# Performance work log

Measured on AMD Instinct MI355X. Metric: run time of the kernel, lower is better.

## Reference

```python
import jax, jax.numpy as jnp
import numpy as np

SEGMENT_LENGTHS = (768, 1536, 3072, 6144, 12288)
DILATED_RATIOS = (1, 2, 4, 8, 16)
NUM_HEADS = 12
NEG_INF = -1e9


def _layer_norm(x, g, b, eps=1e-5):
    mu = jnp.mean(x, axis=-1, keepdims=True)
    var = jnp.mean((x - mu) ** 2, axis=-1, keepdims=True)
    return (x - mu) * jax.lax.rsqrt(var + eps) * g + b


def _dilated_branch(q, k, v, w, r):
    # q,k,v: (B, L, H, Dh); segment length w, dilation ratio r (w % r == 0)
    B, L, H, Dh = q.shape
    Lp = -(-L // w) * w
    n, m = Lp // w, w // r
    gsz = -(-H // r)  # head-group size (heads padded up to a multiple of r in LongNet)
    offs = jnp.arange(H) // gsz  # per-head token offset within each r-block
    oh = jax.nn.one_hot(offs, r, dtype=q.dtype)  # (H, r)

    def gather(t):
        t = jnp.pad(t, ((0, 0), (0, Lp - L), (0, 0), (0, 0)))
        t = t.reshape(B, n, m, r, H, Dh)  # segments of w = m blocks of r
        return jnp.einsum('bnmrhd,hr->bnmhd', t, oh)  # each head picks its offset

    qi, ki, vi = gather(q), gather(k), gather(v)
    s = jnp.einsum('bnihd,bnjhd->bnhij', qi * (Dh ** -0.5), ki)  # (B,n,H,m,m)
    lse = jax.scipy.special.logsumexp(s, axis=-1)  # (B,n,H,m)
    o = jnp.einsum('bnhij,bnjhd->bnihd', jax.nn.softmax(s, axis=-1), vi)
    # scatter back to dense token positions; uncovered slots get 0 / -inf lse
    o_full = jnp.einsum('bnmhd,hr->bnmrhd', o, oh).reshape(B, Lp, H, Dh)
    lse = jnp.transpose(lse, (0, 1, 3, 2))  # (B,n,m,H)
    lse_full = jnp.where(oh.T[None, None, None] > 0, lse[:, :, :, None, :], NEG_INF)
    lse_full = lse_full.reshape(B, Lp, H)
    return o_full[:, :L], lse_full[:, :L]


def _dilated_attention(q, k, v):
    outs, lses = [], []
    for w, r in zip(SEGMENT_LENGTHS, DILATED_RATIOS):
        o, l = _dilated_branch(q, k, v, w, r)
        outs.append(o)
        lses.append(l)
    lse = jnp.stack(lses)  # (n_branch, B, L, H)
    wts = jnp.exp(lse - lse.max(0))
    wts = wts / wts.sum(0)  # softmax-combine branches by their lse (LongNet recombination)
    return (jnp.stack(outs) * wts[..., None]).sum(0)  # (B, L, H, Dh)


def _forward(x, patch_w, patch_b, cls_token, pos_embed,
             ln1_g, ln1_b, wq, bq, wk, bk, wv, bv, wo, bo,
             ln2_g, ln2_b, w1, b1, w2, b2, normf_g, normf_b, head_w, head_b):
    B, Cin, D, Hs, Ws = x.shape
    E = patch_w.shape[0]
    pd, ph, pw = patch_w.shape[2], patch_w.shape[3], patch_w.shape[4]
    # non-overlapping 3D patch embed (Conv3d with stride == kernel)
    xp = x.reshape(B, Cin, D // pd, pd, Hs // ph, ph, Ws // pw, pw)
    tok = jnp.einsum('bcxpyqzr,ecpqr->bxyze', xp, patch_w).reshape(B, -1, E) + patch_b
    tok = tok + pos_embed[:, 1:]
    cls = cls_token + pos_embed[:, :1]
    h = jnp.concatenate([jnp.broadcast_to(cls, (B, 1, E)), tok], axis=1)
    L = h.shape[1]
    Dh = E // NUM_HEADS
    depth = wq.shape[0]
    for i in range(depth):  # pre-LN transformer layers with LongNet dilated attention
        hn = _layer_norm(h, ln1_g[i], ln1_b[i])
        q = (hn @ wq[i] + bq[i]).reshape(B, L, NUM_HEADS, Dh)
        k = (hn @ wk[i] + bk[i]).reshape(B, L, NUM_HEADS, Dh)
        v = (hn @ wv[i] + bv[i]).reshape(B, L, NUM_HEADS, Dh)
        a = _dilated_attention(q, k, v).reshape(B, L, E)
        h = h + a @ wo[i] + bo[i]
        hn = _layer_norm(h, ln2_g[i], ln2_b[i])
        h = h + jax.nn.gelu(hn @ w1[i] + b1[i], approximate=False) @ w2[i] + b2[i]
    h = _layer_norm(h, normf_g, normf_b)
    return h[:, 0] @ head_w + head_b  # (B, num_classes)


def setup_inputs() -> dict:
    key = jax.random.key(0)
    ks = jax.random.split(key, 12)
    B, E, depth, ncls = 2, 768, 2, 1000
    D, Hs, Ws = 48, 256, 256
    N = (D // 4) * (Hs // 16) * (Ws // 16)  # 3072 patches
    f32 = jnp.float32
    s = 0.02
    return {
        'x': jax.random.normal(ks[0], (B, 1, D, Hs, Ws), f32),
        'patch_w': jax.random.normal(ks[1], (E, 1, 4, 16, 16), f32) * s,
        'patch_b': jnp.zeros((E,), f32),
        'cls_token': jax.random.normal(ks[2], (1, 1, E), f32) * s,
        'pos_embed': jax.random.normal(ks[3], (1, N + 1, E), f32) * s,
        'ln1_g': jnp.ones((depth, E), f32),
        'ln1_b': jnp.zeros((depth, E), f32),
        'wq': jax.random.normal(ks[4], (depth, E, E), f32) * s,
        'bq': jnp.zeros((depth, E), f32),
        'wk': jax.random.normal(ks[5], (depth, E, E), f32) * s,
        'bk': jnp.zeros((depth, E), f32),
        'wv': jax.random.normal(ks[6], (depth, E, E), f32) * s,
        'bv': jnp.zeros((depth, E), f32),
        'wo': jax.random.normal(ks[7], (depth, E, E), f32) * s,
        'bo': jnp.zeros((depth, E), f32),
        'ln2_g': jnp.ones((depth, E), f32),
        'ln2_b': jnp.zeros((depth, E), f32),
        'w1': jax.random.normal(ks[8], (depth, E, 4 * E), f32) * s,
        'b1': jnp.zeros((depth, 4 * E), f32),
        'w2': jax.random.normal(ks[9], (depth, 4 * E, E), f32) * s,
        'b2': jnp.zeros((depth, E), f32),
        'normf_g': jnp.ones((E,), f32),
        'normf_b': jnp.zeros((E,), f32),
        'head_w': jax.random.normal(ks[10], (E, ncls), f32) * s,
        'head_b': jnp.zeros((ncls,), f32),
    }


def reference(x, patch_w, patch_b, cls_token, pos_embed,
              ln1_g, ln1_b, wq, bq, wk, bk, wv, bv, wo, bo,
              ln2_g, ln2_b, w1, b1, w2, b2, normf_g, normf_b, head_w, head_b):
    return _forward(x, patch_w, patch_b, cls_token, pos_embed,
                    ln1_g, ln1_b, wq, bq, wk, bk, wv, bv, wo, bo,
                    ln2_g, ln2_b, w1, b1, w2, b2, normf_g, normf_b, head_w, head_b)
```

## Files before the change

kernel.cpp:

```cpp
#include <hip/hip_runtime.h>
#include <math.h>

#define TOK_L 3073
#define EMB 768
#define NH 12
#define DH 64
#define BATCH 2
#define QKVS 2304
#define HSZ ((size_t)BATCH * TOK_L * EMB)
#define MHC ((size_t)BATCH * TOK_L * NH)

typedef __bf16 bf16;
typedef __bf16 v8bf __attribute__((ext_vector_type(8)));
typedef __bf16 v4bf __attribute__((ext_vector_type(4)));
typedef float  v4f  __attribute__((ext_vector_type(4)));

__device__ __forceinline__ v8bf zero8() {
    v8bf v;
    #pragma unroll
    for (int i = 0; i < 8; i++) v[i] = (bf16)0.f;
    return v;
}
__device__ __forceinline__ v4f zero4() {
    v4f v; v[0] = 0.f; v[1] = 0.f; v[2] = 0.f; v[3] = 0.f; return v;
}
__device__ __forceinline__ float gelu_f(float x) {
    return 0.5f * x * (1.0f + erff(x * 0.70710678118654752f));
}
__device__ __forceinline__ void gload16(const bf16* g, bf16* l) {
    __builtin_amdgcn_global_load_lds(
        (const __attribute__((address_space(1))) void*)g,
        (__attribute__((address_space(3))) void*)l, 16, 0, 0);
}

__device__ __forceinline__ void convT_tile(const float* __restrict__ src,
                                           bf16* __restrict__ dst,
                                           int K, int N, int tx, int ty)
{
    __shared__ float t[32][33];
    int n0 = tx * 32, k0 = ty * 32;
    int r = threadIdx.x >> 3, c4 = (threadIdx.x & 7) * 4;
    float4 v = *(const float4*)(src + (size_t)(k0 + r) * N + n0 + c4);
    t[r][c4 + 0] = v.x; t[r][c4 + 1] = v.y; t[r][c4 + 2] = v.z; t[r][c4 + 3] = v.w;
    __syncthreads();
    v4bf o;
    o[0] = (bf16)t[c4 + 0][r]; o[1] = (bf16)t[c4 + 1][r];
    o[2] = (bf16)t[c4 + 2][r]; o[3] = (bf16)t[c4 + 3][r];
    *(v4bf*)(dst + (size_t)(n0 + r) * K + k0 + c4) = o;
}

__global__ __launch_bounds__(256) void prep_weights(
    const float* __restrict__ wq, const float* __restrict__ wk,
    const float* __restrict__ wv, const float* __restrict__ wo,
    const float* __restrict__ w1, const float* __restrict__ w2,
    const float* __restrict__ patch_w,
    bf16* __restrict__ qkv_t0, bf16* __restrict__ wo_t0,
    bf16* __restrict__ w1_t, bf16* __restrict__ w2_t, bf16* __restrict__ pw_b)
{
    int bid = blockIdx.x;
    if (bid >= 13824) {
        int i = ((bid - 13824) * 256 + threadIdx.x) * 4;
        float4 v = *(const float4*)(patch_w + i);
        v4bf o; o[0] = (bf16)v.x; o[1] = (bf16)v.y; o[2] = (bf16)v.z; o[3] = (bf16)v.w;
        *(v4bf*)(pw_b + i) = o;
        return;
    }
    int layer = bid / 6912, t = bid % 6912;
    if (t < 1728) {
        int m = t / 576, tt = t % 576;
        const float* src = (m == 0 ? wq : m == 1 ? wk : wv) + (size_t)layer * 589824;
        bf16* dst = qkv_t0 + (size_t)layer * QKVS * 768 + (size_t)m * 589824;
        convT_tile(src, dst, 768, 768, tt % 24, tt / 24);
    } else if (t < 2304) {
        int tt = t - 1728;
        convT_tile(wo + (size_t)layer * 589824, wo_t0 + (size_t)layer * 589824,
                   768, 768, tt % 24, tt / 24);
    } else if (t < 4608) {
        int tt = t - 2304;
        convT_tile(w1 + (size_t)layer * 2359296, w1_t + (size_t)layer * 2359296,
                   768, 3072, tt % 96, tt / 96);
    } else {
        int tt = t - 4608;
        convT_tile(w2 + (size_t)layer * 2359296, w2_t + (size_t)layer * 2359296,
                   3072, 768, tt % 24, tt / 24);
    }
}

__global__ __launch_bounds__(256) void prep_small(const float* __restrict__ bq,
    const float* __restrict__ bk, const float* __restrict__ bv, float* __restrict__ d,
    const float* __restrict__ cls, const float* __restrict__ pos, float* __restrict__ h)
{
    int i = blockIdx.x * 256 + threadIdx.x;
    if (i < 2 * QKVS) {
        int layer = i / QKVS, j = i % QKVS;
        const float* s = (j < 768) ? bq : (j < 1536) ? bk : bv;
        d[i] = s[(size_t)layer * 768 + (j & 767)];
    }
    if (i < 2 * 768) {
        int b = i / 768, e = i % 768;
        h[(size_t)b * TOK_L * EMB + e] = cls[e] + pos[e];
    }
}

__global__ __launch_bounds__(256) void gather_patches(const float* __restrict__ x,
                                                      bf16* __restrict__ Xp) {
    int p = blockIdx.x;
    int b = p / 3072, pp = p % 3072;
    int px = pp >> 8, py = (pp >> 4) & 15, pz = pp & 15;
    for (int k = threadIdx.x; k < 1024; k += 256) {
        int pd = k >> 8, ph = (k >> 4) & 15, pw = k & 15;
        size_t src = ((size_t)(b * 48 + px * 4 + pd)) * 65536
                   + (size_t)(py * 16 + ph) * 256 + (size_t)(pz * 16 + pw);
        Xp[(size_t)p * 1024 + k] = (bf16)x[src];
    }
}

template<int BN>
__global__ __launch_bounds__(256) void gemm_bf16(
    const bf16* __restrict__ A, const bf16* __restrict__ Bt,
    const float* __restrict__ bias, float* __restrict__ Cf,
    bf16* __restrict__ Cb, int M, int N, int K, int flags,
    const float* __restrict__ pos)
{
    __shared__ bf16 As[128 * 32];
    __shared__ bf16 Bs[BN * 32];
    const int tid = threadIdx.x;
    const int lane = tid & 63, wid = tid >> 6;
    const int ln15 = lane & 15, q4 = lane >> 4;
    const int m0 = blockIdx.y * 128, n0 = blockIdx.x * BN;
    const int wm = (wid & 1) * 64, wn = (wid >> 1) * (BN / 2);
    const int srow = lane >> 2;
    const int schunk = (lane & 3) * 8;
    const int NF = BN / 32;

    v4f acc[4][NF];
    #pragma unroll
    for (int i = 0; i < 4; i++)
        #pragma unroll
        for (int j = 0; j < NF; j++) acc[i][j] = zero4();

    for (int k0 = 0; k0 < K; k0 += 32) {
        #pragma unroll
        for (int i = 0; i < 2; i++) {
            int rg = wid * 32 + i * 16;
            int gm = m0 + rg + srow; if (gm >= M) gm = M - 1;
            gload16(A + (size_t)gm * K + k0 + schunk, As + rg * 32);
        }
        if (BN == 128) {
            #pragma unroll
            for (int i = 0; i < 2; i++) {
                int rg = wid * 32 + i * 16;
                gload16(Bt + (size_t)(n0 + rg + srow) * K + k0 + schunk, Bs + rg * 32);
            }
        } else {
            int rg = wid * 16;
            gload16(Bt + (size_t)(n0 + rg + srow) * K + k0 + schunk, Bs + rg * 32);
        }
        __syncthreads();
        v8bf af[4], bfr[NF];
        #pragma unroll
        for (int mt = 0; mt < 4; mt++)
            af[mt] = *(const v8bf*)(As + (wm + mt * 16 + ln15) * 32 + q4 * 8);
        #pragma unroll
        for (int nt = 0; nt < NF; nt++)
            bfr[nt] = *(const v8bf*)(Bs + (wn + nt * 16 + ln15) * 32 + q4 * 8);
        #pragma unroll
        for (int mt = 0; mt < 4; mt++)
            #pragma unroll
            for (int nt = 0; nt < NF; nt++)
                acc[mt][nt] = __builtin_amdgcn_mfma_f32_16x16x32_bf16(af[mt], bfr[nt], acc[mt][nt], 0, 0, 0);
        __syncthreads();
    }
    #pragma unroll
    for (int mt = 0; mt < 4; mt++) {
        #pragma unroll
        for (int nt = 0; nt < NF; nt++) {
            #pragma unroll
            for (int g = 0; g < 4; g++) {
                int row = m0 + wm + mt * 16 + q4 * 4 + g;
                if (row >= M) continue;
                int col = n0 + wn + nt * 16 + ln15;
                float v = acc[mt][nt][g] + bias[col];
                if (flags & 2) v = gelu_f(v);
                size_t crow;
                if (flags & 4) {
                    int rowp = row % 3072;
                    crow = (size_t)(row + row / 3072 + 1);
                    v += pos[(size_t)(rowp + 1) * EMB + col];
                } else crow = (size_t)row;
                size_t ci = crow * (size_t)N + col;
                if (flags & 8) Cb[ci] = (bf16)v;
                else { if (flags & 1) v += Cf[ci]; Cf[ci] = v; }
            }
        }
    }
}

__global__ __launch_bounds__(256) void layernorm_kernel(
    const float* __restrict__ x, const float* __restrict__ g,
    const float* __restrict__ bb, bf16* __restrict__ y, int nrows)
{
    int row = blockIdx.x;
    if (row >= nrows) return;
    int tid = threadIdx.x;
    const float* xr = x + (size_t)row * EMB;
    float v0 = xr[tid], v1 = xr[tid + 256], v2 = xr[tid + 512];
    __shared__ float red[256];
    red[tid] = v0 + v1 + v2;
    __syncthreads();
    for (int o = 128; o > 0; o >>= 1) { if (tid < o) red[tid] += red[tid + o]; __syncthreads(); }
    float mu = red[0] * (1.f / 768.f);
    __syncthreads();
    float d0 = v0 - mu, d1 = v1 - mu, d2 = v2 - mu;
    red[tid] = d0 * d0 + d1 * d1 + d2 * d2;
    __syncthreads();
    for (int o = 128; o > 0; o >>= 1) { if (tid < o) red[tid] += red[tid + o]; __syncthreads(); }
    float rs = rsqrtf(red[0] * (1.f / 768.f) + 1e-5f);
    bf16* yr = y + (size_t)row * EMB;
    yr[tid]       = (bf16)(d0 * rs * g[tid]       + bb[tid]);
    yr[tid + 256] = (bf16)(d1 * rs * g[tid + 256] + bb[tid + 256]);
    yr[tid + 512] = (bf16)(d2 * rs * g[tid + 512] + bb[tid + 512]);
}

__global__ __launch_bounds__(256) void pack_vt(const bf16* __restrict__ qkv,
                                               bf16* __restrict__ Vt)
{
    __shared__ bf16 t[64 * 65];
    int yy = blockIdx.y;
    int br, seg;
    if (yy < 5)       { br = 0; seg = yy; }
    else if (yy < 8)  { br = 1; seg = yy - 5; }
    else if (yy < 10) { br = 2; seg = yy - 8; }
    else if (yy == 10){ br = 3; seg = 0; }
    else              { br = 4; seg = 0; }
    const int r = 1 << br, w = 768 << br;
    const int gsz = (NH + r - 1) / r;
    const int bh = blockIdx.z;
    const int b = bh / NH, hd = bh % NH;
    const int off = hd / gsz;
    const int kbase = seg * w + off;
    const int kt = blockIdx.x;
    const int tid = threadIdx.x;
    const int dq = (tid & 7) * 8;
    #pragma unroll
    for (int p = 0; p < 2; p++) {
        int jl = (tid >> 3) + p * 32;
        int pk = kbase + (kt * 64 + jl) * r;
        v8bf val = (pk < TOK_L)
            ? *(const v8bf*)(qkv + (size_t)(b * TOK_L + pk) * QKVS + 1536 + hd * DH + dq)
            : zero8();
        #pragma unroll
        for (int i = 0; i < 8; i++) t[jl * 65 + dq + i] = val[i];
    }
    __syncthreads();
    #pragma unroll
    for (int p = 0; p < 2; p++) {
        int d = (tid >> 3) + p * 32;
        int kk = (tid & 7) * 8;
        v8bf o;
        #pragma unroll
        for (int i = 0; i < 8; i++) o[i] = t[(kk + i) * 65 + d];
        *(v8bf*)(Vt + ((size_t)(yy * 24 + bh) * 64 + d) * 768 + kt * 64 + kk) = o;
    }
}

__global__ __launch_bounds__(256) void attn_mfma(
    const bf16* __restrict__ qkv, const bf16* __restrict__ Vt,
    bf16* __restrict__ oac, bf16* __restrict__ obr, float* __restrict__ lse5)
{
    __shared__ bf16 kl[2 * 4096];
    __shared__ bf16 pl[4][32 * 72];
    const int tid = threadIdx.x;
    const int lane = tid & 63, wid = tid >> 6;
    const int ln15 = lane & 15, q4 = lane >> 4;
    const int bid = blockIdx.x;
    const int xcd = bid & 7, rest = bid >> 3;
    const int slot = rest / 6, t = rest - slot * 6;
    const int g = (slot << 3) | xcd;
    const int yy = g / 24, bh = g - yy * 24;
    int br, seg;
    if (yy < 5)       { br = 0; seg = yy; }
    else if (yy < 8)  { br = 1; seg = yy - 5; }
    else if (yy < 10) { br = 2; seg = yy - 8; }
    else if (yy == 10){ br = 3; seg = 0; }
    else              { br = 4; seg = 0; }
    const int r = 1 << br, w = 768 << br;
    const int gsz = (NH + r - 1) / r;
    const int b = bh / NH, hd = bh % NH;
    const int off = hd / gsz;
    const int sbase = seg * w + off;
    if (sbase + (t * 128) * r >= TOK_L) return;

    int n_valid = (TOK_L - sbase + r - 1) / r;
    if (n_valid > 768) n_valid = 768;
    const int kt_lim = (n_valid + 63) >> 6;
    const float pad_add = (float)(768 - n_valid);
    const int qoff = t * 128 + wid * 32;
    const bool wactive = (sbase + qoff * r) < TOK_L;

    const bf16* qb_ = qkv + hd * DH;
    const bf16* kb_ = qkv + 768 + hd * DH;

    auto stageK = [&](int ktv, int bufi) {
        #pragma unroll
        for (int p = 0; p < 2; p++) {
            int row = (tid >> 3) + p * 32;
            int pk = sbase + (ktv * 64 + row) * r;
            if (pk >= TOK_L) pk = 0;
            gload16(kb_ + (size_t)(b * TOK_L + pk) * QKVS + (tid & 7) * 8,
                    kl + bufi * 4096 + wid * 512 + p * 2048);
        }
    };

    v8bf qf[2][2];
    #pragma unroll
    for (int mt = 0; mt < 2; mt++) {
        int pq = sbase + (qoff + mt * 16 + ln15) * r;
        #pragma unroll
        for (int ks = 0; ks < 2; ks++) {
            v8bf qv = (pq < TOK_L)
                ? *(const v8bf*)(qb_ + (size_t)(b * TOK_L + pq) * QKVS + ks * 32 + q4 * 8)
                : zero8();
            #pragma unroll
            for (int i = 0; i < 8; i++) qv[i] = (bf16)((float)qv[i] * 0.125f);
            qf[mt][ks] = qv;
        }
    }
    v4f o[2][4];
    float lsum[2][4];
    #pragma unroll
    for (int mt = 0; mt < 2; mt++)
        #pragma unroll
        for (int g2 = 0; g2 < 4; g2++) { lsum[mt][g2] = 0.f; o[mt][g2] = zero4(); }
    #pragma unroll
    for (int mt = 0; mt < 2; mt++)
        #pragma unroll
        for (int dt = 0; dt < 4; dt++) o[mt][dt] = zero4();

    const bf16* vtb = Vt + (size_t)(yy * 24 + bh) * 64 * 768;
    bf16* plw = &pl[wid][0];

    stageK(0, 0);
    __syncthreads();

    for (int kt = 0; kt < kt_lim; kt++) {
        const int cur = kt & 1;
        if (kt + 1 < kt_lim) stageK(kt + 1, cur ^ 1);
        if (wactive) {
            const bf16* klc = kl + cur * 4096;
            v8bf kf[4][2];
            #pragma unroll
            for (int nt = 0; nt < 4; nt++)
                #pragma unroll
                for (int ks = 0; ks < 2; ks++)
                    kf[nt][ks] = *(const v8bf*)(klc + (nt * 16 + ln15) * 64 + ks * 32 + q4 * 8);
            v4f s[2][4];
            #pragma unroll
            for (int mt = 0; mt < 2; mt++)
                #pragma unroll
                for (int nt = 0; nt < 4; nt++) {
                    s[mt][nt] = __builtin_amdgcn_mfma_f32_16x16x32_bf16(qf[mt][0], kf[nt][0], zero4(), 0, 0, 0);
                    s[mt][nt] = __builtin_amdgcn_mfma_f32_16x16x32_bf16(qf[mt][1], kf[nt][1], s[mt][nt], 0, 0, 0);
                }
            bool vm[4];
            #pragma unroll
            for (int nt = 0; nt < 4; nt++)
                vm[nt] = (kt * 64 + nt * 16 + ln15) < n_valid;
            #pragma unroll
            for (int mt = 0; mt < 2; mt++) {
                #pragma unroll
                for (int g2 = 0; g2 < 4; g2++) {
                    int rowq = mt * 16 + q4 * 4 + g2;
                    #pragma unroll
                    for (int nt = 0; nt < 4; nt++) {
                        float p = vm[nt] ? __expf(s[mt][nt][g2]) : 0.f;
                        lsum[mt][g2] += p;
                        plw[rowq * 72 + nt * 16 + ln15] = (bf16)p;
                    }
                }
            }
            #pragma unroll
            for (int ks = 0; ks < 2; ks++) {
                v8bf pa[2], vf[4];
                #pragma unroll
                for (int mt = 0; mt < 2; mt++)
                    pa[mt] = *(const v8bf*)(plw + (mt * 16 + ln15) * 72 + ks * 32 + q4 * 8);
                #pragma unroll
                for (int dt = 0; dt < 4; dt++)
                    vf[dt] = *(const v8bf*)(vtb + (size_t)(dt * 16 + ln15) * 768 + kt * 64 + ks * 32 + q4 * 8);
                #pragma unroll
                for (int mt = 0; mt < 2; mt++)
                    #pragma unroll
                    for (int dt = 0; dt < 4; dt++)
                        o[mt][dt] = __builtin_amdgcn_mfma_f32_16x16x32_bf16(pa[mt], vf[dt], o[mt][dt], 0, 0, 0);
            }
        }
        __syncthreads();
    }
    if (!wactive) return;

    bf16* od = (br == 0) ? oac : obr + (size_t)(br - 1) * HSZ;
    #pragma unroll
    for (int mt = 0; mt < 2; mt++) {
        #pragma unroll
        for (int g2 = 0; g2 < 4; g2++) {
            float l = lsum[mt][g2];
            l += __shfl_xor(l, 1, 64);
            l += __shfl_xor(l, 2, 64);
            l += __shfl_xor(l, 4, 64);
            l += __shfl_xor(l, 8, 64);
            l += pad_add;
            int row = mt * 16 + q4 * 4 + g2;
            int pq = sbase + (qoff + row) * r;
            if (pq >= TOK_L) continue;
            float linv = 1.f / l;
            if (ln15 == 0)
                lse5[(size_t)br * MHC + (size_t)(b * TOK_L + pq) * NH + hd] = __logf(l);
            #pragma unroll
            for (int dt = 0; dt < 4; dt++)
                od[(size_t)(b * TOK_L + pq) * EMB + hd * DH + dt * 16 + ln15] =
                    (bf16)(o[mt][dt][g2] * linv);
        }
    }
}

__global__ __launch_bounds__(256) void attn_combine(
    const bf16* __restrict__ oac, const bf16* __restrict__ obr,
    const float* __restrict__ lse5, bf16* __restrict__ outb)
{
    size_t e = (size_t)blockIdx.x * 256 + threadIdx.x;
    if (e >= HSZ) return;
    size_t g = e >> 6;
    int h = (int)(g % NH);
    int p = (int)((g / NH) % TOK_L);
    float l0 = lse5[g];
    float m = l0;
    float lv[4];
    bool cov[4];
    #pragma unroll
    for (int j = 0; j < 4; j++) {
        int r = 2 << j;
        int gsz = (NH + r - 1) / r;
        cov[j] = ((p & (r - 1)) == (h / gsz));
        if (cov[j]) {
            lv[j] = lse5[(size_t)(j + 1) * MHC + g];
            m = fmaxf(m, lv[j]);
        }
    }
    float w0 = __expf(l0 - m);
    float wsum = w0;
    float acc = w0 * (float)oac[e];
    #pragma unroll
    for (int j = 0; j < 4; j++) {
        if (cov[j]) {
            float wj = __expf(lv[j] - m);
            wsum += wj;
            acc = fmaf(wj, (float)obr[(size_t)j * HSZ + e], acc);
        }
    }
    outb[e] = (bf16)(acc / wsum);
}

__global__ __launch_bounds__(256) void head_kernel(
    const bf16* __restrict__ hn, const float* __restrict__ hw,
    const float* __restrict__ hb, float* __restrict__ out)
{
    int b = blockIdx.y;
    int c = blockIdx.x * 256 + threadIdx.x;
    __shared__ float srow[EMB];
    for (int e = threadIdx.x; e < EMB; e += 256)
        srow[e] = (float)hn[(size_t)b * TOK_L * EMB + e];
    __syncthreads();
    if (c < 1000) {
        float acc = hb[c];
        for (int e = 0; e < EMB; e++)
            acc = fmaf(srow[e], hw[(size_t)e * 1000 + c], acc);
        out[b * 1000 + c] = acc;
    }
}

extern "C" void kernel_launch(void* const* d_in, const int* in_sizes, int n_in,
                              void* d_out, int out_size, void* d_ws, size_t ws_size,
                              hipStream_t stream)
{
    const float* x       = (const float*)d_in[0];
    const float* patch_w = (const float*)d_in[1];
    const float* patch_b = (const float*)d_in[2];
    const float* cls_tok = (const float*)d_in[3];
    const float* pos_emb = (const float*)d_in[4];
    const float* ln1_g   = (const float*)d_in[5];
    const float* ln1_b   = (const float*)d_in[6];
    const float* wq      = (const float*)d_in[7];
    const float* bq      = (const float*)d_in[8];
    const float* wk      = (const float*)d_in[9];
    const float* bk      = (const float*)d_in[10];
    const float* wv      = (const float*)d_in[11];
    const float* bv      = (const float*)d_in[12];
    const float* wo      = (const float*)d_in[13];
    const float* bo      = (const float*)d_in[14];
    const float* ln2_g   = (const float*)d_in[15];
    const float* ln2_b   = (const float*)d_in[16];
    const float* w1      = (const float*)d_in[17];
    const float* b1      = (const float*)d_in[18];
    const float* w2      = (const float*)d_in[19];
    const float* b2      = (const float*)d_in[20];
    const float* normf_g = (const float*)d_in[21];
    const float* normf_b = (const float*)d_in[22];
    const float* head_w  = (const float*)d_in[23];
    const float* head_b  = (const float*)d_in[24];
    float* out = (float*)d_out;

    char* wp = (char*)d_ws;
    auto alloc = [&](size_t bytes) { char* r = wp; wp += (bytes + 255) & ~(size_t)255; return r; };
    float* h    = (float*)alloc(HSZ * 4);
    bf16*  hn   = (bf16*)alloc(HSZ * 2);
    bf16*  QKV  = (bf16*)alloc((size_t)BATCH * TOK_L * QKVS * 2);
    bf16*  oac  = (bf16*)alloc(HSZ * 2);
    float* lse5 = (float*)alloc(5 * MHC * 4);
    bf16*  Vt   = (bf16*)alloc((size_t)12 * 24 * 64 * 768 * 2);
    bf16*  mid  = (bf16*)alloc(4 * HSZ * 2);
    bf16*  obr  = mid;
    bf16*  Xp   = mid;

    bf16*  qkv_t0 = (bf16*)alloc((size_t)2 * QKVS * 768 * 2);
    bf16*  wo_t0  = (bf16*)alloc((size_t)2 * 768 * 768 * 2);
    bf16*  w1_t   = (bf16*)alloc((size_t)2 * 3072 * 768 * 2);
    bf16*  w2_t   = (bf16*)alloc((size_t)2 * 768 * 3072 * 2);
    bf16*  pw_b   = (bf16*)alloc((size_t)768 * 1024 * 2);
    float* bqkv   = (float*)alloc((size_t)2 * QKVS * 4);

    const int M = BATCH * TOK_L;
    const int MT = (M + 127) / 128;

    prep_weights<<<dim3(14592), 256, 0, stream>>>(wq, wk, wv, wo, w1, w2, patch_w,
                                                  qkv_t0, wo_t0, w1_t, w2_t, pw_b);
    prep_small<<<dim3(18), 256, 0, stream>>>(bq, bk, bv, bqkv, cls_tok, pos_emb, h);

    gather_patches<<<dim3(BATCH * 3072), 256, 0, stream>>>(x, Xp);
    gemm_bf16<64><<<dim3(12, 48), 256, 0, stream>>>(Xp, pw_b, patch_b, h, nullptr,
                                                    BATCH * 3072, 768, 1024, 4, pos_emb);

    for (int layer = 0; layer < 2; layer++) {
        size_t bOff  = (size_t)layer * 768;
        size_t b1Off = (size_t)layer * 3072;
        bf16* qt   = qkv_t0 + (size_t)layer * QKVS * 768;
        bf16* wo_t = wo_t0 + (size_t)layer * 589824;

        layernorm_kernel<<<dim3(M), 256, 0, stream>>>(h, ln1_g + bOff, ln1_b + bOff, hn, M);
        gemm_bf16<128><<<dim3(18, MT), 256, 0, stream>>>(hn, qt, bqkv + (size_t)layer * QKVS,
                                                         nullptr, QKV, M, QKVS, 768, 8, nullptr);

        pack_vt<<<dim3(12, 12, 24), 256, 0, stream>>>(QKV, Vt);
        attn_mfma<<<dim3(1728), 256, 0, stream>>>(QKV, Vt, oac, obr, lse5);
        attn_combine<<<dim3((unsigned)((HSZ + 255) / 256)), 256, 0, stream>>>(oac, obr, lse5, hn);

        gemm_bf16<64><<<dim3(12, MT), 256, 0, stream>>>(hn, wo_t, bo + bOff, h, nullptr,
                                                        M, 768, 768, 1, nullptr);

        layernorm_kernel<<<dim3(M), 256, 0, stream>>>(h, ln2_g + bOff, ln2_b + bOff, hn, M);
        gemm_bf16<128><<<dim3(24, MT), 256, 0, stream>>>(hn, w1_t + (size_t)layer * 2359296, b1 + b1Off,
                                                         nullptr, mid, M, 3072, 768, 8 | 2, nullptr);
        gemm_bf16<64><<<dim3(12, MT), 256, 0, stream>>>(mid, w2_t + (size_t)layer * 2359296, b2 + bOff,
                                                        h, nullptr, M, 768, 3072, 1, nullptr);
    }

    layernorm_kernel<<<dim3(M), 256, 0, stream>>>(h, normf_g, normf_b, hn, M);
    head_kernel<<<dim3(4, BATCH), 256, 0, stream>>>(hn, head_w, head_b, out);
}
```

Baseline: 1.054 ms.

## Use fragment-major LDS layouts, XCD-aware GEMM tile mapping, and exp2 softmax

```diff
diff --git a/kernel.cpp b/kernel.cpp
--- a/kernel.cpp
+++ b/kernel.cpp
@@ -120,18 +120,21 @@
     const bf16* __restrict__ A, const bf16* __restrict__ Bt,
     const float* __restrict__ bias, float* __restrict__ Cf,
     bf16* __restrict__ Cb, int M, int N, int K, int flags,
-    const float* __restrict__ pos)
+    const float* __restrict__ pos, int NT)
 {
     __shared__ bf16 As[128 * 32];
     __shared__ bf16 Bs[BN * 32];
     const int tid = threadIdx.x;
     const int lane = tid & 63, wid = tid >> 6;
     const int ln15 = lane & 15, q4 = lane >> 4;
-    const int m0 = blockIdx.y * 128, n0 = blockIdx.x * BN;
+    const int idx = blockIdx.x >> 3, xcd = blockIdx.x & 7;
+    const int m_idx = (idx / NT) * 8 + xcd;
+    const int n_idx = idx % NT;
+    const int m0 = m_idx * 128, n0 = n_idx * BN;
+    if (m0 >= M) return;
     const int wm = (wid & 1) * 64, wn = (wid >> 1) * (BN / 2);
-    const int srow = lane >> 2;
-    const int schunk = (lane & 3) * 8;
     const int NF = BN / 32;
+    const int lrow = lane & 15, lchunk = lane >> 4;
 
     v4f acc[4][NF];
     #pragma unroll
@@ -141,29 +144,28 @@
 
     for (int k0 = 0; k0 < K; k0 += 32) {
         #pragma unroll
-        for (int i = 0; i < 2; i++) {
-            int rg = wid * 32 + i * 16;
-            int gm = m0 + rg + srow; if (gm >= M) gm = M - 1;
-            gload16(A + (size_t)gm * K + k0 + schunk, As + rg * 32);
+        for (int fi = 0; fi < 2; fi++) {
+            int f = wid * 2 + fi;
+            int gm = m0 + f * 16 + lrow; if (gm >= M) gm = M - 1;
+            gload16(A + (size_t)gm * K + k0 + lchunk * 8, As + f * 512);
         }
         if (BN == 128) {
             #pragma unroll
-            for (int i = 0; i < 2; i++) {
-                int rg = wid * 32 + i * 16;
-                gload16(Bt + (size_t)(n0 + rg + srow) * K + k0 + schunk, Bs + rg * 32);
+            for (int fi = 0; fi < 2; fi++) {
+                int f = wid * 2 + fi;
+                gload16(Bt + (size_t)(n0 + f * 16 + lrow) * K + k0 + lchunk * 8, Bs + f * 512);
             }
         } else {
-            int rg = wid * 16;
-            gload16(Bt + (size_t)(n0 + rg + srow) * K + k0 + schunk, Bs + rg * 32);
+            gload16(Bt + (size_t)(n0 + wid * 16 + lrow) * K + k0 + lchunk * 8, Bs + wid * 512);
         }
         __syncthreads();
         v8bf af[4], bfr[NF];
         #pragma unroll
         for (int mt = 0; mt < 4; mt++)
-            af[mt] = *(const v8bf*)(As + (wm + mt * 16 + ln15) * 32 + q4 * 8);
+            af[mt] = *(const v8bf*)(As + ((wid & 1) * 4 + mt) * 512 + lane * 8);
         #pragma unroll
         for (int nt = 0; nt < NF; nt++)
-            bfr[nt] = *(const v8bf*)(Bs + (wn + nt * 16 + ln15) * 32 + q4 * 8);
+            bfr[nt] = *(const v8bf*)(Bs + ((wid >> 1) * NF + nt) * 512 + lane * 8);
         #pragma unroll
         for (int mt = 0; mt < 4; mt++)
             #pragma unroll
@@ -253,14 +255,18 @@
         for (int i = 0; i < 8; i++) t[jl * 65 + dq + i] = val[i];
     }
     __syncthreads();
+    size_t base = ((size_t)(yy * 24 + bh) * 12 + kt) * 4096;
     #pragma unroll
     for (int p = 0; p < 2; p++) {
-        int d = (tid >> 3) + p * 32;
-        int kk = (tid & 7) * 8;
+        int cc = p * 256 + tid;
+        int f = cc >> 6, lanei = cc & 63;
+        int dt = f >> 1, ks = f & 1;
+        int dh = dt * 16 + (lanei & 15);
+        int k0e = ks * 32 + (lanei >> 4) * 8;
         v8bf o;
         #pragma unroll
-        for (int i = 0; i < 8; i++) o[i] = t[(kk + i) * 65 + d];
-        *(v8bf*)(Vt + ((size_t)(yy * 24 + bh) * 64 + d) * 768 + kt * 64 + kk) = o;
+        for (int i = 0; i < 8; i++) o[i] = t[(k0e + i) * 65 + dh];
+        *(v8bf*)(Vt + base + (size_t)cc * 8) = o;
     }
 }
 
@@ -269,10 +275,11 @@
     bf16* __restrict__ oac, bf16* __restrict__ obr, float* __restrict__ lse5)
 {
     __shared__ bf16 kl[2 * 4096];
-    __shared__ bf16 pl[4][32 * 72];
+    __shared__ bf16 pl[4][2048];
     const int tid = threadIdx.x;
     const int lane = tid & 63, wid = tid >> 6;
     const int ln15 = lane & 15, q4 = lane >> 4;
+    const int lrow = lane & 15, lchunk = lane >> 4;
     const int bid = blockIdx.x;
     const int xcd = bid & 7, rest = bid >> 3;
     const int slot = rest / 6, t = rest - slot * 6;
@@ -303,15 +310,16 @@
 
     auto stageK = [&](int ktv, int bufi) {
         #pragma unroll
-        for (int p = 0; p < 2; p++) {
-            int row = (tid >> 3) + p * 32;
-            int pk = sbase + (ktv * 64 + row) * r;
+        for (int fi = 0; fi < 2; fi++) {
+            int f = wid * 2 + fi;
+            int pk = sbase + (ktv * 64 + (f >> 1) * 16 + lrow) * r;
             if (pk >= TOK_L) pk = 0;
-            gload16(kb_ + (size_t)(b * TOK_L + pk) * QKVS + (tid & 7) * 8,
-                    kl + bufi * 4096 + wid * 512 + p * 2048);
+            gload16(kb_ + (size_t)(b * TOK_L + pk) * QKVS + (f & 1) * 32 + lchunk * 8,
+                    kl + bufi * 4096 + f * 512);
         }
     };
 
+    const float qscale = 0.125f * 1.44269504088896f;
     v8bf qf[2][2];
     #pragma unroll
     for (int mt = 0; mt < 2; mt++) {
@@ -322,7 +330,7 @@
                 ? *(const v8bf*)(qb_ + (size_t)(b * TOK_L + pq) * QKVS + ks * 32 + q4 * 8)
                 : zero8();
             #pragma unroll
-            for (int i = 0; i < 8; i++) qv[i] = (bf16)((float)qv[i] * 0.125f);
+            for (int i = 0; i < 8; i++) qv[i] = (bf16)((float)qv[i] * qscale);
             qf[mt][ks] = qv;
         }
     }
@@ -331,13 +339,13 @@
     #pragma unroll
     for (int mt = 0; mt < 2; mt++)
         #pragma unroll
-        for (int g2 = 0; g2 < 4; g2++) { lsum[mt][g2] = 0.f; o[mt][g2] = zero4(); }
+        for (int g2 = 0; g2 < 4; g2++) lsum[mt][g2] = 0.f;
     #pragma unroll
     for (int mt = 0; mt < 2; mt++)
         #pragma unroll
         for (int dt = 0; dt < 4; dt++) o[mt][dt] = zero4();
 
-    const bf16* vtb = Vt + (size_t)(yy * 24 + bh) * 64 * 768;
+    const bf16* vtb = Vt + (size_t)(yy * 24 + bh) * 12 * 4096;
     bf16* plw = &pl[wid][0];
 
     stageK(0, 0);
@@ -353,7 +361,7 @@
             for (int nt = 0; nt < 4; nt++)
                 #pragma unroll
                 for (int ks = 0; ks < 2; ks++)
-                    kf[nt][ks] = *(const v8bf*)(klc + (nt * 16 + ln15) * 64 + ks * 32 + q4 * 8);
+                    kf[nt][ks] = *(const v8bf*)(klc + (nt * 2 + ks) * 512 + lane * 8);
             v4f s[2][4];
             #pragma unroll
             for (int mt = 0; mt < 2; mt++)
@@ -370,12 +378,13 @@
             for (int mt = 0; mt < 2; mt++) {
                 #pragma unroll
                 for (int g2 = 0; g2 < 4; g2++) {
-                    int rowq = mt * 16 + q4 * 4 + g2;
+                    int rowq4 = q4 * 4 + g2;
                     #pragma unroll
                     for (int nt = 0; nt < 4; nt++) {
-                        float p = vm[nt] ? __expf(s[mt][nt][g2]) : 0.f;
+                        float p = vm[nt] ? exp2f(s[mt][nt][g2]) : 0.f;
                         lsum[mt][g2] += p;
-                        plw[rowq * 72 + nt * 16 + ln15] = (bf16)p;
+                        int q4p = (nt * 2 + (ln15 >> 3)) & 3;
+                        plw[((mt * 2 + (nt >> 1)) << 9) + ((q4p * 16 + rowq4) << 3) + (ln15 & 7)] = (bf16)p;
                     }
                 }
             }
@@ -384,10 +393,10 @@
                 v8bf pa[2], vf[4];
                 #pragma unroll
                 for (int mt = 0; mt < 2; mt++)
-                    pa[mt] = *(const v8bf*)(plw + (mt * 16 + ln15) * 72 + ks * 32 + q4 * 8);
+                    pa[mt] = *(const v8bf*)(plw + ((mt * 2 + ks) << 9) + lane * 8);
                 #pragma unroll
                 for (int dt = 0; dt < 4; dt++)
-                    vf[dt] = *(const v8bf*)(vtb + (size_t)(dt * 16 + ln15) * 768 + kt * 64 + ks * 32 + q4 * 8);
+                    vf[dt] = *(const v8bf*)(vtb + (size_t)kt * 4096 + (dt * 2 + ks) * 512 + lane * 8);
                 #pragma unroll
                 for (int mt = 0; mt < 2; mt++)
                     #pragma unroll
@@ -517,7 +526,7 @@
     bf16*  QKV  = (bf16*)alloc((size_t)BATCH * TOK_L * QKVS * 2);
     bf16*  oac  = (bf16*)alloc(HSZ * 2);
     float* lse5 = (float*)alloc(5 * MHC * 4);
-    bf16*  Vt   = (bf16*)alloc((size_t)12 * 24 * 64 * 768 * 2);
+    bf16*  Vt   = (bf16*)alloc((size_t)12 * 24 * 12 * 4096 * 2);
     bf16*  mid  = (bf16*)alloc(4 * HSZ * 2);
     bf16*  obr  = mid;
     bf16*  Xp   = mid;
@@ -530,15 +539,16 @@
     float* bqkv   = (float*)alloc((size_t)2 * QKVS * 4);
 
     const int M = BATCH * TOK_L;
-    const int MT = (M + 127) / 128;
+    const int MTp = (((M + 127) / 128 + 7) / 8) * 8;
+    const int MTe = 48;
 
     prep_weights<<<dim3(14592), 256, 0, stream>>>(wq, wk, wv, wo, w1, w2, patch_w,
                                                   qkv_t0, wo_t0, w1_t, w2_t, pw_b);
     prep_small<<<dim3(18), 256, 0, stream>>>(bq, bk, bv, bqkv, cls_tok, pos_emb, h);
 
     gather_patches<<<dim3(BATCH * 3072), 256, 0, stream>>>(x, Xp);
-    gemm_bf16<64><<<dim3(12, 48), 256, 0, stream>>>(Xp, pw_b, patch_b, h, nullptr,
-                                                    BATCH * 3072, 768, 1024, 4, pos_emb);
+    gemm_bf16<64><<<dim3(12 * MTe), 256, 0, stream>>>(Xp, pw_b, patch_b, h, nullptr,
+                                                      BATCH * 3072, 768, 1024, 4, pos_emb, 12);
 
     for (int layer = 0; layer < 2; layer++) {
         size_t bOff  = (size_t)layer * 768;
@@ -547,21 +557,21 @@
         bf16* wo_t = wo_t0 + (size_t)layer * 589824;
 
         layernorm_kernel<<<dim3(M), 256, 0, stream>>>(h, ln1_g + bOff, ln1_b + bOff, hn, M);
-        gemm_bf16<128><<<dim3(18, MT), 256, 0, stream>>>(hn, qt, bqkv + (size_t)layer * QKVS,
-                                                         nullptr, QKV, M, QKVS, 768, 8, nullptr);
+        gemm_bf16<128><<<dim3(18 * MTp), 256, 0, stream>>>(hn, qt, bqkv + (size_t)layer * QKVS,
+                                                           nullptr, QKV, M, QKVS, 768, 8, nullptr, 18);
 
         pack_vt<<<dim3(12, 12, 24), 256, 0, stream>>>(QKV, Vt);
         attn_mfma<<<dim3(1728), 256, 0, stream>>>(QKV, Vt, oac, obr, lse5);
         attn_combine<<<dim3((unsigned)((HSZ + 255) / 256)), 256, 0, stream>>>(oac, obr, lse5, hn);
 
-        gemm_bf16<64><<<dim3(12, MT), 256, 0, stream>>>(hn, wo_t, bo + bOff, h, nullptr,
-                                                        M, 768, 768, 1, nullptr);
+        gemm_bf16<64><<<dim3(12 * MTp), 256, 0, stream>>>(hn, wo_t, bo + bOff, h, nullptr,
+                                                          M, 768, 768, 1, nullptr, 12);
 
         layernorm_kernel<<<dim3(M), 256, 0, stream>>>(h, ln2_g + bOff, ln2_b + bOff, hn, M);
-        gemm_bf16<128><<<dim3(24, MT), 256, 0, stream>>>(hn, w1_t + (size_t)layer * 2359296, b1 + b1Off,
-                                                         nullptr, mid, M, 3072, 768, 8 | 2, nullptr);
-        gemm_bf16<64><<<dim3(12, MT), 256, 0, stream>>>(mid, w2_t + (size_t)layer * 2359296, b2 + bOff,
-                                                        h, nullptr, M, 768, 3072, 1, nullptr);
+        gemm_bf16<128><<<dim3(24 * MTp), 256, 0, stream>>>(hn, w1_t + (size_t)layer * 2359296, b1 + b1Off,
+                                                           nullptr, mid, M, 3072, 768, 8 | 2, nullptr, 24);
+        gemm_bf16<64><<<dim3(12 * MTp), 256, 0, stream>>>(mid, w2_t + (size_t)layer * 2359296, b2 + bOff,
+                                                          h, nullptr, M, 768, 3072, 1, nullptr, 12);
     }
 
     layernorm_kernel<<<dim3(M), 256, 0, stream>>>(h, normf_g, normf_b, hn, M);
```

Result: slower. 1.175 ms (+11.4%).
